# Performance work log

Hardware: AMD Instinct MI355X
Metric: run time of the kernel (lower is better)

## Reference

```python
import jax, jax.numpy as jnp
import numpy as np

N_NODES = 100000
N_EDGES = 1600000
N_GRAPHS = 256


def gcn_conv(x, src, dst, edge_weight, W, b, num_nodes):
    """PyG GCNConv: add self-loops, symmetric degree normalization,
    linear transform, scatter-add aggregation, bias."""
    loop = jnp.arange(num_nodes)
    s = jnp.concatenate([src, loop])
    d = jnp.concatenate([dst, loop])
    ew = jnp.concatenate([edge_weight, jnp.ones((num_nodes,), dtype=edge_weight.dtype)])
    deg = jax.ops.segment_sum(ew, d, num_segments=num_nodes)  # [N]
    dinv = jnp.where(deg > 0, deg ** -0.5, 0.0)
    norm = dinv[s] * ew * dinv[d]  # [E+N]
    h = x @ W  # [N, out]
    msg = h[s] * norm[:, None]  # gather + scale
    out = jax.ops.segment_sum(msg, d, num_segments=num_nodes)  # scatter-add
    return out + b


def global_mean_pool(x, batch, num_graphs):
    s = jax.ops.segment_sum(x, batch, num_segments=num_graphs)
    cnt = jax.ops.segment_sum(jnp.ones((x.shape[0],), dtype=x.dtype), batch, num_segments=num_graphs)
    return s / jnp.maximum(cnt, 1.0)[:, None]


def setup_inputs() -> dict:
    key = jax.random.key(0)
    ks = jax.random.split(key, 12)
    x = jax.random.normal(ks[0], (N_NODES, 128), dtype=jnp.float32)
    edge_index = jax.random.randint(ks[1], (2, N_EDGES), 0, N_NODES, dtype=jnp.int64)
    edge_attr = jax.random.uniform(ks[2], (N_EDGES,), dtype=jnp.float32)
    batch = jnp.sort(jax.random.randint(ks[3], (N_NODES,), 0, N_GRAPHS, dtype=jnp.int64))
    def lin(k, fan_in, fan_out):
        lim = 1.0 / np.sqrt(fan_in)
        kw, kb = jax.random.split(k)
        W = jax.random.uniform(kw, (fan_in, fan_out), minval=-lim, maxval=lim, dtype=jnp.float32)
        b = jax.random.uniform(kb, (fan_out,), minval=-lim, maxval=lim, dtype=jnp.float32)
        return W, b
    W1, b1 = lin(ks[4], 128, 64)
    W2, b2 = lin(ks[5], 64, 64)
    W3, b3 = lin(ks[6], 64, 64)
    Wl, bl = lin(ks[7], 64, 10)
    return {"x": x, "edge_index": edge_index, "edge_attr": edge_attr, "batch": batch,
            "W1": W1, "b1": b1, "W2": W2, "b2": b2, "W3": W3, "b3": b3, "Wl": Wl, "bl": bl}


def reference(x, edge_index, edge_attr, batch, W1, b1, W2, b2, W3, b3, Wl, bl):
    src, dst = edge_index[0], edge_index[1]
    n = x.shape[0]
    h = jax.nn.relu(gcn_conv(x, src, dst, edge_attr, W1, b1, n))
    h = jax.nn.relu(gcn_conv(h, src, dst, edge_attr, W2, b2, n))
    h = jax.nn.relu(gcn_conv(h, src, dst, edge_attr, W3, b3, n))
    g = global_mean_pool(h, batch, N_GRAPHS)  # [G, 64]
    return g @ Wl + bl  # [G, num_classes]
```

## Files before the change

### kernel.cpp

```cpp
#include <hip/hip_runtime.h>
#include <hip/hip_bf16.h>

#define N_NODES  100000
#define N_EDGES  1600000
#define N_GRAPHS 256
#define F 64
#define NBUCK  782
#define NCHUNK 782


__global__ __launch_bounds__(256) void k_hist(const int* __restrict__ dst, int* __restrict__ hist) {
    __shared__ int lh[NBUCK];
    int tid = threadIdx.x, chunk = blockIdx.x;
    for (int j = tid; j < NBUCK; j += 256) lh[j] = 0;
    __syncthreads();
    int e0 = chunk * 2048;
#pragma unroll
    for (int i = 0; i < 8; i++) {
        int e = e0 + i * 256 + tid;
        if (e < N_EDGES) atomicAdd(&lh[dst[e] >> 7], 1);
    }
    __syncthreads();
    for (int j = tid; j < NBUCK; j += 256) hist[chunk * NBUCK + j] = lh[j];
}

__global__ __launch_bounds__(256) void k_colscan(int* __restrict__ hist, int* __restrict__ btot) {
    __shared__ int ts[256];
    int b = blockIdx.x, tid = threadIdx.x;
    int v[4], loc[4], run = 0;
#pragma unroll
    for (int k = 0; k < 4; k++) {
        int c = tid * 4 + k;
        v[k] = (c < NCHUNK) ? hist[c * NBUCK + b] : 0;
        loc[k] = run; run += v[k];
    }
    ts[tid] = run;
    __syncthreads();
    int x = run;
    for (int off = 1; off < 256; off <<= 1) {
        int t = (tid >= off) ? ts[tid - off] : 0;
        __syncthreads();
        x += t; ts[tid] = x;
        __syncthreads();
    }
    int texcl = x - run;
#pragma unroll
    for (int k = 0; k < 4; k++) {
        int c = tid * 4 + k;
        if (c < NCHUNK) hist[c * NBUCK + b] = texcl + loc[k];
    }
    if (tid == 255) btot[b] = x;
}

__global__ __launch_bounds__(256) void k_bscan(const int* __restrict__ btot, int* __restrict__ base) {
    __shared__ int ts[256];
    int tid = threadIdx.x;
    int v[4], loc[4], run = 0;
#pragma unroll
    for (int k = 0; k < 4; k++) {
        int c = tid * 4 + k;
        v[k] = (c < NBUCK) ? btot[c] : 0;
        loc[k] = run; run += v[k];
    }
    ts[tid] = run;
    __syncthreads();
    int x = run;
    for (int off = 1; off < 256; off <<= 1) {
        int t = (tid >= off) ? ts[tid - off] : 0;
        __syncthreads();
        x += t; ts[tid] = x;
        __syncthreads();
    }
    int texcl = x - run;
#pragma unroll
    for (int k = 0; k < 4; k++) {
        int c = tid * 4 + k;
        if (c < NBUCK) base[c] = texcl + loc[k];
    }
    if (tid == 255) base[NBUCK] = x;
}

__global__ __launch_bounds__(256) void k_partition(const int* __restrict__ src, const int* __restrict__ dst,
                                                   const float* __restrict__ ew,
                                                   const int* __restrict__ hist, const int* __restrict__ base,
                                                   long long* __restrict__ part) {
    __shared__ int cursor[NBUCK];
    int tid = threadIdx.x, chunk = blockIdx.x;
    for (int j = tid; j < NBUCK; j += 256) cursor[j] = base[j] + hist[chunk * NBUCK + j];
    __syncthreads();
    int e0 = chunk * 2048;
#pragma unroll
    for (int i = 0; i < 8; i++) {
        int e = e0 + i * 256 + tid;
        if (e < N_EDGES) {
            int d = dst[e];
            int pos = atomicAdd(&cursor[d >> 7], 1);
            unsigned lo = (unsigned)src[e] | ((unsigned)(d & 127) << 17);
            long long rec = (long long)((unsigned long long)lo |
                            ((unsigned long long)__float_as_uint(ew[e]) << 32));
            part[pos] = rec;
        }
    }
}

__global__ __launch_bounds__(256) void k_bucket(const long long* __restrict__ part,
                                                const int* __restrict__ base,
                                                float* __restrict__ dinv_g, int* __restrict__ row_off,
                                                int2* __restrict__ esec) {
    __shared__ float fdeg[128];
    __shared__ float sdinv[128];
    __shared__ int   cnt[128];
    __shared__ int   sc[128];
    __shared__ int   cursor[128];
    int b = blockIdx.x, tid = threadIdx.x;
    if (tid < 128) { fdeg[tid] = 1.0f; cnt[tid] = 0; }
    __syncthreads();
    int e0 = base[b], e1 = base[b + 1], ne = e1 - e0;
    for (int k = tid; k < ne; k += 256) {
        long long rec = part[e0 + k];
        int lo = (int)rec;
        int d7 = (lo >> 17) & 127;
        atomicAdd(&fdeg[d7], __uint_as_float((unsigned)(rec >> 32)));
        atomicAdd(&cnt[d7], 1);
    }
    __syncthreads();
    int myc = 0, x = 0;
    if (tid < 128) {
        float dv = rsqrtf(fdeg[tid]);
        sdinv[tid] = dv;
        int node = b * 128 + tid;
        if (node < N_NODES) dinv_g[node] = dv;
        myc = cnt[tid]; x = myc; sc[tid] = x;
    }
    __syncthreads();
    for (int off = 1; off < 128; off <<= 1) {
        int t = (tid < 128 && tid >= off) ? sc[tid - off] : 0;
        __syncthreads();
        if (tid < 128) { x += t; sc[tid] = x; }
        __syncthreads();
    }
    if (tid < 128) {
        int excl = x - myc;
        int node = b * 128 + tid;
        if (node < N_NODES) row_off[node] = e0 + excl;
        cursor[tid] = e0 + excl;
    }
    if (b == 0 && tid == 0) row_off[N_NODES] = N_EDGES;
    __syncthreads();
    for (int k = tid; k < ne; k += 256) {
        long long rec = part[e0 + k];
        int lo = (int)rec;
        int d7 = (lo >> 17) & 127;
        float w = __uint_as_float((unsigned)(rec >> 32));
        int pos = atomicAdd(&cursor[d7], 1);
        esec[pos] = make_int2((lo & 0x1FFFF) << 7, __float_as_int(w * sdinv[d7]));
    }
}

__global__ void k_coef(int2* __restrict__ esec, const float* __restrict__ dinv_g) {
    int e = blockIdx.x * 256 + threadIdx.x;
    if (e < N_EDGES) {
        int2 v = esec[e];
        esec[e] = make_int2(v.x, __float_as_int(__int_as_float(v.y) * dinv_g[((unsigned)v.x) >> 7]));
    } else if (e < N_EDGES + 16) {
        esec[e] = make_int2(0, 0);
    }
}

__global__ void k_gstart(const int* __restrict__ batch, int* gstart) {
    int g = blockIdx.x * 256 + threadIdx.x;
    if (g > N_GRAPHS) return;
    int lo = 0, hi = N_NODES;
    while (lo < hi) {
        int mid = (lo + hi) >> 1;
        if (batch[mid] < g) lo = mid + 1; else hi = mid;
    }
    gstart[g] = lo;
}

template <int K>
__global__ __launch_bounds__(256) void k_gemm(const float* __restrict__ X,
                                              const float* __restrict__ W,
                                              __hip_bfloat16* __restrict__ H) {
    constexpr int KC = 32;
    constexpr int XP = KC + 4;
    __shared__ float Xs[128 * XP];
    __shared__ float Ws[KC * F];
    const int tid  = threadIdx.x;
    const int fgrp = tid & 15;
    const int ngrp = tid >> 4;
    const int f0   = fgrp * 4;
    const int nb   = blockIdx.x * 128;

    float acc[8][4];
#pragma unroll
    for (int i = 0; i < 8; i++)
#pragma unroll
        for (int j = 0; j < 4; j++) acc[i][j] = 0.0f;

    for (int kc = 0; kc < K; kc += KC) {
        if (kc) __syncthreads();
#pragma unroll
        for (int pass = 0; pass < 4; pass++) {
            int idx = tid + pass * 256;
            int r = idx >> 3, q = idx & 7;
            int gr = nb + r; if (gr >= N_NODES) gr = N_NODES - 1;
            float4 v = *(const float4*)&X[(size_t)gr * K + kc + q * 4];
            *(float4*)&Xs[r * XP + q * 4] = v;
        }
#pragma unroll
        for (int pass = 0; pass < 2; pass++) {
            int idx = tid + pass * 256;
            float4 v = *(const float4*)&W[(size_t)(kc + (idx >> 4)) * F + (idx & 15) * 4];
            *(float4*)&Ws[idx * 4] = v;
        }
        __syncthreads();
#pragma unroll
        for (int k = 0; k < KC; k += 4) {
            float4 wv[4];
#pragma unroll
            for (int kk = 0; kk < 4; kk++)
                wv[kk] = *(const float4*)&Ws[(k + kk) * F + f0];
#pragma unroll
            for (int i = 0; i < 8; i++) {
                float4 xv = *(const float4*)&Xs[(ngrp + 16 * i) * XP + k];
                acc[i][0] = fmaf(xv.x, wv[0].x, acc[i][0]);
                acc[i][0] = fmaf(xv.y, wv[1].x, acc[i][0]);
                acc[i][0] = fmaf(xv.z, wv[2].x, acc[i][0]);
                acc[i][0] = fmaf(xv.w, wv[3].x, acc[i][0]);
                acc[i][1] = fmaf(xv.x, wv[0].y, acc[i][1]);
                acc[i][1] = fmaf(xv.y, wv[1].y, acc[i][1]);
                acc[i][1] = fmaf(xv.z, wv[2].y, acc[i][1]);
                acc[i][1] = fmaf(xv.w, wv[3].y, acc[i][1]);
                acc[i][2] = fmaf(xv.x, wv[0].z, acc[i][2]);
                acc[i][2] = fmaf(xv.y, wv[1].z, acc[i][2]);
                acc[i][2] = fmaf(xv.z, wv[2].z, acc[i][2]);
                acc[i][2] = fmaf(xv.w, wv[3].z, acc[i][2]);
                acc[i][3] = fmaf(xv.x, wv[0].w, acc[i][3]);
                acc[i][3] = fmaf(xv.y, wv[1].w, acc[i][3]);
                acc[i][3] = fmaf(xv.z, wv[2].w, acc[i][3]);
                acc[i][3] = fmaf(xv.w, wv[3].w, acc[i][3]);
            }
        }
    }
#pragma unroll
    for (int i = 0; i < 8; i++) {
        int gn = nb + ngrp + 16 * i;
        if (gn < N_NODES) {
            __hip_bfloat16 hb[4];
            hb[0] = __float2bfloat16(acc[i][0]);
            hb[1] = __float2bfloat16(acc[i][1]);
            hb[2] = __float2bfloat16(acc[i][2]);
            hb[3] = __float2bfloat16(acc[i][3]);
            *(uint2*)&H[(size_t)gn * F + f0] = *(uint2*)hb;
        }
    }
}

__global__ __launch_bounds__(256) void k_agg(const __hip_bfloat16* __restrict__ H,
                                             const int* __restrict__ row_off,
                                             const long long* __restrict__ esec,
                                             const float* __restrict__ dinv,
                                             const float* __restrict__ bias,
                                             float* __restrict__ O) {
    int node = blockIdx.x * 4 + (threadIdx.x >> 6);
    int lane = threadIdx.x & 63;
    int beg = __builtin_amdgcn_readfirstlane(row_off[node]);
    int end = __builtin_amdgcn_readfirstlane(row_off[node + 1]);
    float di = dinv[node];
    const char* Hb = (const char*)H + lane * 2;
    float hself = __bfloat162float(H[(size_t)node * F + lane]);
    float base = bias[lane] + di * di * hself;
    float a[16];
#pragma unroll
    for (int u = 0; u < 16; u++) a[u] = 0.0f;
    for (int j = beg; j < end; j += 16) {
        long long e[16];
#pragma unroll
        for (int u = 0; u < 16; u++) e[u] = esec[j + u];
#pragma unroll
        for (int u = 0; u < 16; u++) {
            unsigned off = (unsigned)(int)e[u];
            float c = (j + u < end) ? __int_as_float((int)(e[u] >> 32)) : 0.0f;
            float hv = __bfloat162float(*(const __hip_bfloat16*)(Hb + off));
            a[u] = fmaf(c, hv, a[u]);
        }
    }
    float s0 = ((a[0] + a[1]) + (a[2] + a[3])) + ((a[4] + a[5]) + (a[6] + a[7]));
    float s1 = ((a[8] + a[9]) + (a[10] + a[11])) + ((a[12] + a[13]) + (a[14] + a[15]));
    O[(size_t)node * F + lane] = fmaxf(base + s0 + s1, 0.0f);
}

__global__ __launch_bounds__(256) void k_pool_linear(const float* __restrict__ H,
                                                     const int* __restrict__ gstart,
                                                     const float* __restrict__ Wl,
                                                     const float* __restrict__ bl,
                                                     float* __restrict__ out) {
    int g = blockIdx.x;
    int beg = gstart[g], end = gstart[g + 1];
    int lane = threadIdx.x & 63, wv = threadIdx.x >> 6;
    float acc = 0.0f;
    for (int r = beg + wv; r < end; r += 4)
        acc += H[(size_t)r * F + lane];
    __shared__ float s[4][F];
    s[wv][lane] = acc;
    __syncthreads();
    if (wv == 0) {
        float tot = s[0][lane] + s[1][lane] + s[2][lane] + s[3][lane];
        float cntf = (float)(end - beg);
        float p = tot / fmaxf(cntf, 1.0f);
        for (int c = 0; c < 10; c++) {
            float v = p * Wl[lane * 10 + c];
            for (int off = 32; off; off >>= 1) v += __shfl_down(v, off);
            if (lane == 0) out[g * 10 + c] = v + bl[c];
        }
    }
}


extern "C" void kernel_launch(void* const* d_in, const int* in_sizes, int n_in,
                              void* d_out, int out_size, void* d_ws, size_t ws_size,
                              hipStream_t stream) {
    const float* x    = (const float*)d_in[0];
    const int*   ei   = (const int*)d_in[1];
    const float* ea   = (const float*)d_in[2];
    const int*   bat  = (const int*)d_in[3];
    const float* W1   = (const float*)d_in[4];
    const float* b1   = (const float*)d_in[5];
    const float* W2   = (const float*)d_in[6];
    const float* b2   = (const float*)d_in[7];
    const float* W3   = (const float*)d_in[8];
    const float* b3   = (const float*)d_in[9];
    const float* Wl   = (const float*)d_in[10];
    const float* bl   = (const float*)d_in[11];
    float* out = (float*)d_out;

    const int* src = ei;
    const int* dst = ei + N_EDGES;

    char* ws = (char*)d_ws;
    size_t off = 0;
    auto carve = [&](size_t bytes) {
        void* p = ws + off;
        off += (bytes + 255) & ~(size_t)255;
        return p;
    };
    float*          dinv    = (float*)carve(N_NODES * 4);
    int*            row_off = (int*)  carve((N_NODES + 1) * 4);
    int2*           esec    = (int2*) carve(((size_t)N_EDGES + 16) * 8);
    __hip_bfloat16* hbuf    = (__hip_bfloat16*)carve((size_t)N_NODES * F * 2);
    float*          obuf    = (float*)carve((size_t)N_NODES * F * 4);
    int*            gstart  = (int*)  carve((N_GRAPHS + 1) * 4);
    (void)ws_size; (void)in_sizes; (void)n_in; (void)out_size;

    long long* part = (long long*)hbuf;
    char* alias = (char*)obuf;
    int* hist = (int*)alias;                         alias += (size_t)NCHUNK * NBUCK * 4;
    int* btot = (int*)alias;                         alias += (NBUCK + 8) * 4;
    int* base = (int*)alias;

    const int EB  = (N_EDGES + 255) / 256 + 1;
    const int GB  = (N_NODES + 127) / 128;

    k_hist     <<<NCHUNK, 256, 0, stream>>>(dst, hist);
    k_colscan  <<<NBUCK,  256, 0, stream>>>(hist, btot);
    k_bscan    <<<1,      256, 0, stream>>>(btot, base);
    k_partition<<<NCHUNK, 256, 0, stream>>>(src, dst, ea, hist, base, part);
    k_bucket   <<<NBUCK,  256, 0, stream>>>(part, base, dinv, row_off, esec);
    k_coef     <<<EB,     256, 0, stream>>>(esec, dinv);
    k_gstart   <<<2,      256, 0, stream>>>(bat, gstart);

    k_gemm<128><<<GB, 256, 0, stream>>>(x, W1, hbuf);
    k_agg<<<N_NODES / 4, 256, 0, stream>>>(hbuf, row_off, (const long long*)esec, dinv, b1, obuf);
    k_gemm<64><<<GB, 256, 0, stream>>>(obuf, W2, hbuf);
    k_agg<<<N_NODES / 4, 256, 0, stream>>>(hbuf, row_off, (const long long*)esec, dinv, b2, obuf);
    k_gemm<64><<<GB, 256, 0, stream>>>(obuf, W3, hbuf);
    k_agg<<<N_NODES / 4, 256, 0, stream>>>(hbuf, row_off, (const long long*)esec, dinv, b3, obuf);

    k_pool_linear<<<N_GRAPHS, 256, 0, stream>>>(obuf, gstart, Wl, bl, out);
}
```

Baseline: 421.4 us.

## Vectorize aggregation gathers per edge and store layer outputs as bf16

The aggregation kernel now has each group of 8 lanes fetch a whole 128-byte bf16 row per edge with 16-byte loads. Eight edges are processed in parallel per wavefront and combined with cross-lane shuffle reductions, replacing the previous 2-byte per-lane gathers. Layer outputs are written as bf16 rather than fp32, so the following GEMM and the pooling kernel read half the bytes; the GEMM gains a bf16-input path. The extra bf16 rounding of intermediate activations changes numerics slightly, and the shuffle reduction adds ALU work.

```diff
diff --git a/kernel.cpp b/kernel.cpp
--- a/kernel.cpp
+++ b/kernel.cpp
@@ -178,8 +178,8 @@
     gstart[g] = lo;
 }
 
-template <int K>
-__global__ __launch_bounds__(256) void k_gemm(const float* __restrict__ X,
+template <int K, bool BF16IN>
+__global__ __launch_bounds__(256) void k_gemm(const void* __restrict__ Xv,
                                               const float* __restrict__ W,
                                               __hip_bfloat16* __restrict__ H) {
     constexpr int KC = 32;
@@ -200,13 +200,34 @@
 
     for (int kc = 0; kc < K; kc += KC) {
         if (kc) __syncthreads();
-#pragma unroll
-        for (int pass = 0; pass < 4; pass++) {
-            int idx = tid + pass * 256;
-            int r = idx >> 3, q = idx & 7;
-            int gr = nb + r; if (gr >= N_NODES) gr = N_NODES - 1;
-            float4 v = *(const float4*)&X[(size_t)gr * K + kc + q * 4];
-            *(float4*)&Xs[r * XP + q * 4] = v;
+        if (BF16IN) {
+            const unsigned short* X = (const unsigned short*)Xv;
+#pragma unroll
+            for (int pass = 0; pass < 2; pass++) {
+                int idx = tid + pass * 256;
+                int r = idx >> 2, q = idx & 3;
+                int gr = nb + r; if (gr >= N_NODES) gr = N_NODES - 1;
+                uint4 v = *(const uint4*)&X[(size_t)gr * K + kc + q * 8];
+                float* dp = &Xs[r * XP + q * 8];
+                dp[0] = __uint_as_float(v.x << 16);
+                dp[1] = __uint_as_float(v.x & 0xffff0000u);
+                dp[2] = __uint_as_float(v.y << 16);
+                dp[3] = __uint_as_float(v.y & 0xffff0000u);
+                dp[4] = __uint_as_float(v.z << 16);
+                dp[5] = __uint_as_float(v.z & 0xffff0000u);
+                dp[6] = __uint_as_float(v.w << 16);
+                dp[7] = __uint_as_float(v.w & 0xffff0000u);
+            }
+        } else {
+            const float* X = (const float*)Xv;
+#pragma unroll
+            for (int pass = 0; pass < 4; pass++) {
+                int idx = tid + pass * 256;
+                int r = idx >> 3, q = idx & 7;
+                int gr = nb + r; if (gr >= N_NODES) gr = N_NODES - 1;
+                float4 v = *(const float4*)&X[(size_t)gr * K + kc + q * 4];
+                *(float4*)&Xs[r * XP + q * 4] = v;
+            }
         }
 #pragma unroll
         for (int pass = 0; pass < 2; pass++) {
@@ -259,39 +280,72 @@
 
 __global__ __launch_bounds__(256) void k_agg(const __hip_bfloat16* __restrict__ H,
                                              const int* __restrict__ row_off,
-                                             const long long* __restrict__ esec,
+                                             const int2* __restrict__ esec,
                                              const float* __restrict__ dinv,
                                              const float* __restrict__ bias,
-                                             float* __restrict__ O) {
+                                             __hip_bfloat16* __restrict__ O) {
     int node = blockIdx.x * 4 + (threadIdx.x >> 6);
     int lane = threadIdx.x & 63;
+    int q  = lane >> 3;
+    int f8 = lane & 7;
     int beg = __builtin_amdgcn_readfirstlane(row_off[node]);
     int end = __builtin_amdgcn_readfirstlane(row_off[node + 1]);
-    float di = dinv[node];
-    const char* Hb = (const char*)H + lane * 2;
-    float hself = __bfloat162float(H[(size_t)node * F + lane]);
-    float base = bias[lane] + di * di * hself;
-    float a[16];
-#pragma unroll
-    for (int u = 0; u < 16; u++) a[u] = 0.0f;
-    for (int j = beg; j < end; j += 16) {
-        long long e[16];
-#pragma unroll
-        for (int u = 0; u < 16; u++) e[u] = esec[j + u];
-#pragma unroll
-        for (int u = 0; u < 16; u++) {
-            unsigned off = (unsigned)(int)e[u];
-            float c = (j + u < end) ? __int_as_float((int)(e[u] >> 32)) : 0.0f;
-            float hv = __bfloat162float(*(const __hip_bfloat16*)(Hb + off));
-            a[u] = fmaf(c, hv, a[u]);
-        }
-    }
-    float s0 = ((a[0] + a[1]) + (a[2] + a[3])) + ((a[4] + a[5]) + (a[6] + a[7]));
-    float s1 = ((a[8] + a[9]) + (a[10] + a[11])) + ((a[12] + a[13]) + (a[14] + a[15]));
-    O[(size_t)node * F + lane] = fmaxf(base + s0 + s1, 0.0f);
-}
-
-__global__ __launch_bounds__(256) void k_pool_linear(const float* __restrict__ H,
+    const char* Hbase = (const char*)H;
+
+    float a[8];
+#pragma unroll
+    for (int u = 0; u < 8; u++) a[u] = 0.0f;
+
+    for (int j = beg; j < end; j += 8) {
+        int2 ev = esec[j + q];
+        float c = (j + q < end) ? __int_as_float(ev.y) : 0.0f;
+        uint4 hq = *(const uint4*)(Hbase + (unsigned)ev.x + (f8 << 4));
+        a[0] = fmaf(c, __uint_as_float(hq.x << 16),         a[0]);
+        a[1] = fmaf(c, __uint_as_float(hq.x & 0xffff0000u), a[1]);
+        a[2] = fmaf(c, __uint_as_float(hq.y << 16),         a[2]);
+        a[3] = fmaf(c, __uint_as_float(hq.y & 0xffff0000u), a[3]);
+        a[4] = fmaf(c, __uint_as_float(hq.z << 16),         a[4]);
+        a[5] = fmaf(c, __uint_as_float(hq.z & 0xffff0000u), a[5]);
+        a[6] = fmaf(c, __uint_as_float(hq.w << 16),         a[6]);
+        a[7] = fmaf(c, __uint_as_float(hq.w & 0xffff0000u), a[7]);
+    }
+#pragma unroll
+    for (int m = 8; m < 64; m <<= 1) {
+#pragma unroll
+        for (int u = 0; u < 8; u++) a[u] += __shfl_xor(a[u], m);
+    }
+    if (q == 0) {
+        float di = dinv[node];
+        float di2 = di * di;
+        uint4 hs = *(const uint4*)(Hbase + (size_t)node * 128 + (f8 << 4));
+        float hv[8];
+        hv[0] = __uint_as_float(hs.x << 16);
+        hv[1] = __uint_as_float(hs.x & 0xffff0000u);
+        hv[2] = __uint_as_float(hs.y << 16);
+        hv[3] = __uint_as_float(hs.y & 0xffff0000u);
+        hv[4] = __uint_as_float(hs.z << 16);
+        hv[5] = __uint_as_float(hs.z & 0xffff0000u);
+        hv[6] = __uint_as_float(hs.w << 16);
+        hv[7] = __uint_as_float(hs.w & 0xffff0000u);
+        const float4* bp = (const float4*)(bias + f8 * 8);
+        float4 b0 = bp[0], b1 = bp[1];
+        float r[8];
+        r[0] = fmaxf(a[0] + b0.x + di2 * hv[0], 0.0f);
+        r[1] = fmaxf(a[1] + b0.y + di2 * hv[1], 0.0f);
+        r[2] = fmaxf(a[2] + b0.z + di2 * hv[2], 0.0f);
+        r[3] = fmaxf(a[3] + b0.w + di2 * hv[3], 0.0f);
+        r[4] = fmaxf(a[4] + b1.x + di2 * hv[4], 0.0f);
+        r[5] = fmaxf(a[5] + b1.y + di2 * hv[5], 0.0f);
+        r[6] = fmaxf(a[6] + b1.z + di2 * hv[6], 0.0f);
+        r[7] = fmaxf(a[7] + b1.w + di2 * hv[7], 0.0f);
+        __hip_bfloat16 hb[8];
+#pragma unroll
+        for (int u = 0; u < 8; u++) hb[u] = __float2bfloat16(r[u]);
+        *(uint4*)&O[(size_t)node * F + f8 * 8] = *(uint4*)hb;
+    }
+}
+
+__global__ __launch_bounds__(256) void k_pool_linear(const __hip_bfloat16* __restrict__ H,
                                                      const int* __restrict__ gstart,
                                                      const float* __restrict__ Wl,
                                                      const float* __restrict__ bl,
@@ -301,7 +355,7 @@
     int lane = threadIdx.x & 63, wv = threadIdx.x >> 6;
     float acc = 0.0f;
     for (int r = beg + wv; r < end; r += 4)
-        acc += H[(size_t)r * F + lane];
+        acc += __bfloat162float(H[(size_t)r * F + lane]);
     __shared__ float s[4][F];
     s[wv][lane] = acc;
     __syncthreads();
@@ -349,12 +403,12 @@
     int*            row_off = (int*)  carve((N_NODES + 1) * 4);
     int2*           esec    = (int2*) carve(((size_t)N_EDGES + 16) * 8);
     __hip_bfloat16* hbuf    = (__hip_bfloat16*)carve((size_t)N_NODES * F * 2);
-    float*          obuf    = (float*)carve((size_t)N_NODES * F * 4);
+    __hip_bfloat16* obuf    = (__hip_bfloat16*)carve((size_t)N_NODES * F * 4);
     int*            gstart  = (int*)  carve((N_GRAPHS + 1) * 4);
     (void)ws_size; (void)in_sizes; (void)n_in; (void)out_size;
 
     long long* part = (long long*)hbuf;
-    char* alias = (char*)obuf;
+    char* alias = (char*)obuf + (size_t)N_NODES * F * 2;
     int* hist = (int*)alias;                         alias += (size_t)NCHUNK * NBUCK * 4;
     int* btot = (int*)alias;                         alias += (NBUCK + 8) * 4;
     int* base = (int*)alias;
@@ -370,12 +424,12 @@
     k_coef     <<<EB,     256, 0, stream>>>(esec, dinv);
     k_gstart   <<<2,      256, 0, stream>>>(bat, gstart);
 
-    k_gemm<128><<<GB, 256, 0, stream>>>(x, W1, hbuf);
-    k_agg<<<N_NODES / 4, 256, 0, stream>>>(hbuf, row_off, (const long long*)esec, dinv, b1, obuf);
-    k_gemm<64><<<GB, 256, 0, stream>>>(obuf, W2, hbuf);
-    k_agg<<<N_NODES / 4, 256, 0, stream>>>(hbuf, row_off, (const long long*)esec, dinv, b2, obuf);
-    k_gemm<64><<<GB, 256, 0, stream>>>(obuf, W3, hbuf);
-    k_agg<<<N_NODES / 4, 256, 0, stream>>>(hbuf, row_off, (const long long*)esec, dinv, b3, obuf);
+    k_gemm<128, false><<<GB, 256, 0, stream>>>(x, W1, hbuf);
+    k_agg<<<N_NODES / 4, 256, 0, stream>>>(hbuf, row_off, esec, dinv, b1, obuf);
+    k_gemm<64, true><<<GB, 256, 0, stream>>>(obuf, W2, hbuf);
+    k_agg<<<N_NODES / 4, 256, 0, stream>>>(hbuf, row_off, esec, dinv, b2, obuf);
+    k_gemm<64, true><<<GB, 256, 0, stream>>>(obuf, W3, hbuf);
+    k_agg<<<N_NODES / 4, 256, 0, stream>>>(hbuf, row_off, esec, dinv, b3, obuf);
 
     k_pool_linear<<<N_GRAPHS, 256, 0, stream>>>(obuf, gstart, Wl, bl, out);
 }
```

Result: no change. 418.8 us (-0.6%).
